# Kernel tuning notes

Hardware: AMD Instinct MI355X
Metric: run time of the kernel (lower is better)

Reference implementation:

```python
import jax, jax.numpy as jnp
import numpy as np

N_NODES = 100000
N_EDGES = 3200000
N_GRAPHS = 256
DIMS = [38, 64, 32, 16]


def setup_inputs() -> dict:
    key = jax.random.key(0)
    ks = jax.random.split(key, 16)
    x = jax.random.normal(ks[0], (N_NODES, DIMS[0]), dtype=jnp.float32)
    edge_index = jax.random.randint(ks[1], (2, N_EDGES), 0, N_NODES, dtype=jnp.int64)
    batch_vec = jnp.sort(jax.random.randint(ks[2], (N_NODES,), 0, N_GRAPHS, dtype=jnp.int64))
    inp = {"x": x, "edge_index": edge_index, "batch_vec": batch_vec}
    # Per layer l: W_rel [out,in] (with bias b [out]), W_root [out,in] (no bias)
    ki = 3
    for l in range(3):
        din, dout = DIMS[l], DIMS[l + 1]
        s = 1.0 / np.sqrt(din)
        inp[f"W_rel{l}"] = jax.random.uniform(ks[ki], (dout, din), minval=-s, maxval=s, dtype=jnp.float32); ki += 1
        inp[f"b{l}"] = jax.random.uniform(ks[ki], (dout,), minval=-s, maxval=s, dtype=jnp.float32); ki += 1
        inp[f"W_root{l}"] = jax.random.uniform(ks[ki], (dout, din), minval=-s, maxval=s, dtype=jnp.float32); ki += 1
    return inp


def _graph_conv(x, src, dst, W_rel, b, W_root):
    # sum_{j -> i} x_j, then linear (equivalent to summing transformed messages)
    agg = jax.ops.segment_sum(x[src], dst, num_segments=N_NODES)  # [N, din]
    return agg @ W_rel.T + b + x @ W_root.T


def reference(x, edge_index, batch_vec, W_rel0, b0, W_root0, W_rel1, b1, W_root1, W_rel2, b2, W_root2):
    src, dst = edge_index[0], edge_index[1]
    h = jnp.tanh(_graph_conv(x, src, dst, W_rel0, b0, W_root0))
    h = jnp.tanh(_graph_conv(h, src, dst, W_rel1, b1, W_root1))
    h = _graph_conv(h, src, dst, W_rel2, b2, W_root2)
    # global mean pool over graphs
    sums = jax.ops.segment_sum(h, batch_vec, num_segments=N_GRAPHS)  # [G, 16]
    counts = jax.ops.segment_sum(jnp.ones((N_NODES,), dtype=h.dtype), batch_vec, num_segments=N_GRAPHS)
    pooled = sums / jnp.maximum(counts, 1.0)[:, None]
    return jnp.tanh(pooled)
```

## Files before the change

### kernel.cpp

```cpp
#include <hip/hip_runtime.h>
#include <math.h>

#define N_NODES  100000
#define N_EDGES  3200000
#define N_GRAPHS 256


#define BSHIFT 8
#define NB ((N_NODES + 255) >> 8)
#define NBLK 640
#define EPB ((N_EDGES + NBLK - 1) / NBLK)

__device__ __forceinline__ float fast_tanh(float x) {
    x = fminf(20.f, fmaxf(-20.f, x));
    float e = __expf(2.f * x);
    return (e - 1.f) / (e + 1.f);
}

__device__ __forceinline__ unsigned int pack_bf2(float a, float b) {
    unsigned int ua = __float_as_uint(a);
    unsigned int ub = __float_as_uint(b);
    ua += 0x7fffu + ((ua >> 16) & 1u);
    ub += 0x7fffu + ((ub >> 16) & 1u);
    return (ua >> 16) | (ub & 0xffff0000u);
}


__global__ __launch_bounds__(256) void k_hist(const int* __restrict__ dst,
                                              int* __restrict__ bucket_cnt,
                                              int* __restrict__ blockoff) {
    __shared__ int hist[NB];
    int tid = threadIdx.x;
    int b = blockIdx.x;
    for (int i = tid; i < NB; i += 256) hist[i] = 0;
    __syncthreads();
    int lo = b * EPB;
    int hi = min(lo + EPB, N_EDGES);
    for (int e = lo + tid; e < hi; e += 256)
        atomicAdd(&hist[dst[e] >> BSHIFT], 1);
    __syncthreads();
    for (int i = tid; i < NB; i += 256) {
        int c = hist[i];
        blockoff[b * NB + i] = (c > 0) ? atomicAdd(&bucket_cnt[i], c) : 0;
    }
}

__global__ __launch_bounds__(512) void k_scan_buckets(const int* __restrict__ bucket_cnt,
                                                      int* __restrict__ bucket_base) {
    __shared__ int sd[512];
    int tid = threadIdx.x;
    int v = (tid < NB) ? bucket_cnt[tid] : 0;
    int val = v;
    sd[tid] = val;
    __syncthreads();
#pragma unroll
    for (int off = 1; off < 512; off <<= 1) {
        int t = (tid >= off) ? sd[tid - off] : 0;
        __syncthreads();
        val += t;
        sd[tid] = val;
        __syncthreads();
    }
    if (tid < NB) {
        bucket_base[tid] = val - v;
        if (tid == NB - 1) bucket_base[NB] = val;
    }
}

__global__ __launch_bounds__(256) void k_scatter_buckets(const int* __restrict__ src,
                                                         const int* __restrict__ dst,
                                                         const int* __restrict__ bucket_base,
                                                         const int* __restrict__ blockoff,
                                                         int* __restrict__ ebuf) {
    __shared__ int base[NB];
    __shared__ int cur[NB];
    int tid = threadIdx.x;
    int b = blockIdx.x;
    for (int i = tid; i < NB; i += 256) {
        base[i] = bucket_base[i] + blockoff[b * NB + i];
        cur[i] = 0;
    }
    __syncthreads();
    int lo = b * EPB;
    int hi = min(lo + EPB, N_EDGES);
    for (int e = lo + tid; e < hi; e += 256) {
        int d = dst[e];
        int bin = d >> BSHIFT;
        int r = atomicAdd(&cur[bin], 1);
        ebuf[base[bin] + r] = src[e] | ((d & 255) << 17);
    }
}

__global__ __launch_bounds__(256) void k_bucket_csr(const int* __restrict__ ebuf,
                                                    const int* __restrict__ bucket_base,
                                                    int* __restrict__ rowptr,
                                                    int* __restrict__ rowend,
                                                    int* __restrict__ elist) {
    __shared__ int cnt[256];
    __shared__ int nb[256];
    __shared__ int cur[256];
    __shared__ int sscan[256];
    int b = blockIdx.x;
    int tid = threadIdx.x;
    int e0 = bucket_base[b];
    int e1 = bucket_base[b + 1];
    cnt[tid] = 0;
    cur[tid] = 0;
    __syncthreads();
    for (int j = e0 + tid; j < e1; j += 256)
        atomicAdd(&cnt[ebuf[j] >> 17], 1);
    __syncthreads();
    int v = cnt[tid];
    int val = v;
    sscan[tid] = val;
    __syncthreads();
#pragma unroll
    for (int off = 1; off < 256; off <<= 1) {
        int t = (tid >= off) ? sscan[tid - off] : 0;
        __syncthreads();
        val += t;
        sscan[tid] = val;
        __syncthreads();
    }
    int excl = val - v;
    nb[tid] = excl;
    int node = (b << BSHIFT) + tid;
    if (node < N_NODES) {
        rowptr[node] = e0 + excl;
        rowend[node] = e0 + val;
    }
    __syncthreads();
    for (int j = e0 + tid; j < e1; j += 256) {
        int w = ebuf[j];
        int dl = w >> 17;
        int r = atomicAdd(&cur[dl], 1);
        elist[e0 + nb[dl] + r] = w & 0x1FFFF;
    }
}

__global__ __launch_bounds__(256) void k_cast_bf16(const float* __restrict__ in,
                                                   unsigned int* __restrict__ out,
                                                   int n_pairs) {
    int i = blockIdx.x * 256 + threadIdx.x;
    if (i >= n_pairs) return;
    float2 v = ((const float2*)in)[i];
    out[i] = pack_bf2(v.x, v.y);
}

template<int DIM2>
__global__ __launch_bounds__(256) void k_gather_bf16(const unsigned int* __restrict__ feat,
                                                     const int* __restrict__ rowptr,
                                                     const int* __restrict__ rowend,
                                                     const int* __restrict__ elist,
                                                     float* __restrict__ agg) {
    int idx = blockIdx.x * 256 + threadIdx.x;
    if (idx >= N_NODES * DIM2) return;
    int n = idx / DIM2;
    int p = idx - n * DIM2;
    int j = rowptr[n];
    int e = rowend[n];
    float a0 = 0.f, a1 = 0.f;
    for (; j + 3 < e; j += 4) {
        int s0 = elist[j];
        int s1 = elist[j + 1];
        int s2 = elist[j + 2];
        int s3 = elist[j + 3];
        unsigned int w0 = feat[s0 * DIM2 + p];
        unsigned int w1 = feat[s1 * DIM2 + p];
        unsigned int w2 = feat[s2 * DIM2 + p];
        unsigned int w3 = feat[s3 * DIM2 + p];
        a0 += __uint_as_float(w0 << 16);
        a1 += __uint_as_float(w0 & 0xffff0000u);
        a0 += __uint_as_float(w1 << 16);
        a1 += __uint_as_float(w1 & 0xffff0000u);
        a0 += __uint_as_float(w2 << 16);
        a1 += __uint_as_float(w2 & 0xffff0000u);
        a0 += __uint_as_float(w3 << 16);
        a1 += __uint_as_float(w3 & 0xffff0000u);
    }
    for (; j < e; ++j) {
        unsigned int w = feat[elist[j] * DIM2 + p];
        a0 += __uint_as_float(w << 16);
        a1 += __uint_as_float(w & 0xffff0000u);
    }
    agg[n * (2 * DIM2) + 2 * p]     = a0;
    agg[n * (2 * DIM2) + 2 * p + 1] = a1;
}

__global__ __launch_bounds__(256) void k_fused0(const float* __restrict__ agg,
                                                const float* __restrict__ x,
                                                const float* __restrict__ Wrel0,
                                                const float* __restrict__ b0,
                                                const float* __restrict__ Wroot0,
                                                const float* __restrict__ Wrel1,
                                                const float* __restrict__ b1,
                                                const float* __restrict__ Wroot1,
                                                unsigned int* __restrict__ y1b,
                                                float* __restrict__ r1) {
    __shared__ float sWr[64 * 40];
    __shared__ float sWt[64 * 40];
    __shared__ float sW1r[64 * 32];
    __shared__ float sW1t[64 * 32];
    __shared__ float sb0[64];
    __shared__ float sb1[32];
    int tid = threadIdx.x;
    for (int i = tid; i < 64 * 40; i += 256) {
        int o = i / 40, d = i - o * 40;
        sWr[i] = (d < 38) ? Wrel0[o * 38 + d] : 0.f;
        sWt[i] = (d < 38) ? Wroot0[o * 38 + d] : 0.f;
    }
    for (int i = tid; i < 64 * 32; i += 256) {
        int k = i >> 5, j = i & 31;
        sW1r[i] = Wrel1[j * 64 + k];
        sW1t[i] = Wroot1[j * 64 + k];
    }
    if (tid < 64) sb0[tid] = b0[tid];
    if (tid < 32) sb1[tid] = b1[tid];
    __syncthreads();

    int n = blockIdx.x * 256 + tid;
    if (n >= N_NODES) return;

    float xa[40], xx[40];
    const float2* a2 = (const float2*)(agg + (size_t)n * 38);
    const float2* x2 = (const float2*)(x + (size_t)n * 38);
#pragma unroll
    for (int i = 0; i < 19; ++i) {
        float2 va = a2[i]; xa[2 * i] = va.x; xa[2 * i + 1] = va.y;
        float2 vx = x2[i]; xx[2 * i] = vx.x; xx[2 * i + 1] = vx.y;
    }
    xa[38] = xa[39] = 0.f;
    xx[38] = xx[39] = 0.f;

    float y1[32], rr[32];
#pragma unroll
    for (int j = 0; j < 32; ++j) { y1[j] = 0.f; rr[j] = sb1[j]; }

#pragma unroll 4
    for (int o = 0; o < 64; ++o) {
        float acc = sb0[o];
        const float4* wr = (const float4*)(sWr + o * 40);
        const float4* wt = (const float4*)(sWt + o * 40);
#pragma unroll
        for (int d = 0; d < 10; ++d) {
            float4 a = wr[d], b = wt[d];
            acc += xa[4 * d] * a.x + xa[4 * d + 1] * a.y + xa[4 * d + 2] * a.z + xa[4 * d + 3] * a.w;
            acc += xx[4 * d] * b.x + xx[4 * d + 1] * b.y + xx[4 * d + 2] * b.z + xx[4 * d + 3] * b.w;
        }
        float h = fast_tanh(acc);
        const float4* w1 = (const float4*)(sW1r + o * 32);
        const float4* w2 = (const float4*)(sW1t + o * 32);
#pragma unroll
        for (int j = 0; j < 8; ++j) {
            float4 a = w1[j], b = w2[j];
            y1[4 * j]     += h * a.x; y1[4 * j + 1] += h * a.y;
            y1[4 * j + 2] += h * a.z; y1[4 * j + 3] += h * a.w;
            rr[4 * j]     += h * b.x; rr[4 * j + 1] += h * b.y;
            rr[4 * j + 2] += h * b.z; rr[4 * j + 3] += h * b.w;
        }
    }

    unsigned int* yo = y1b + (size_t)n * 16;
#pragma unroll
    for (int p = 0; p < 16; ++p) yo[p] = pack_bf2(y1[2 * p], y1[2 * p + 1]);
    float4* ro = (float4*)(r1 + (size_t)n * 32);
#pragma unroll
    for (int j = 0; j < 8; ++j) ro[j] = make_float4(rr[4 * j], rr[4 * j + 1], rr[4 * j + 2], rr[4 * j + 3]);
}

__global__ __launch_bounds__(256) void k_fused1(const float* __restrict__ agg,
                                                const float* __restrict__ r1,
                                                const float* __restrict__ Wrel2,
                                                float* __restrict__ h2,
                                                unsigned int* __restrict__ y2b)
{
    __shared__ float sW[32 * 16];
    int tid = threadIdx.x;
    for (int i = tid; i < 512; i += 256) {
        int k = i >> 4, j = i & 15;
        sW[i] = Wrel2[j * 32 + k];
    }
    __syncthreads();
    int n = blockIdx.x * 256 + tid;
    if (n >= N_NODES) return;
    const float4* a4 = (const float4*)(agg + (size_t)n * 32);
    const float4* r4 = (const float4*)(r1 + (size_t)n * 32);
    float h[32];
#pragma unroll
    for (int i = 0; i < 8; ++i) {
        float4 a = a4[i], r = r4[i];
        h[4 * i]     = fast_tanh(a.x + r.x);
        h[4 * i + 1] = fast_tanh(a.y + r.y);
        h[4 * i + 2] = fast_tanh(a.z + r.z);
        h[4 * i + 3] = fast_tanh(a.w + r.w);
    }
    float4* ho = (float4*)(h2 + (size_t)n * 32);
#pragma unroll
    for (int i = 0; i < 8; ++i) ho[i] = make_float4(h[4 * i], h[4 * i + 1], h[4 * i + 2], h[4 * i + 3]);
    float y[16];
#pragma unroll
    for (int j = 0; j < 16; ++j) y[j] = 0.f;
#pragma unroll
    for (int k = 0; k < 32; ++k) {
        const float4* w = (const float4*)(sW + k * 16);
#pragma unroll
        for (int j = 0; j < 4; ++j) {
            float4 wv = w[j];
            y[4 * j]     += h[k] * wv.x; y[4 * j + 1] += h[k] * wv.y;
            y[4 * j + 2] += h[k] * wv.z; y[4 * j + 3] += h[k] * wv.w;
        }
    }
    unsigned int* yo = y2b + (size_t)n * 8;
#pragma unroll
    for (int p = 0; p < 8; ++p) yo[p] = pack_bf2(y[2 * p], y[2 * p + 1]);
}

__global__ __launch_bounds__(256) void k_graph_start(const int* __restrict__ batch,
                                                     int* __restrict__ gstart) {
    int i = blockIdx.x * 256 + threadIdx.x;
    if (i >= N_NODES) return;
    int g = batch[i];
    int gp = (i == 0) ? -1 : batch[i - 1];
    for (int gg = gp + 1; gg <= g; ++gg) gstart[gg] = i;
    if (i == N_NODES - 1)
        for (int gg = g + 1; gg <= N_GRAPHS; ++gg) gstart[gg] = N_NODES;
}

__global__ __launch_bounds__(256) void k_pool(const float* __restrict__ agg,
                                              const float* __restrict__ h2,
                                              const int* __restrict__ gstart,
                                              float* __restrict__ psum)
{
    __shared__ float part[4][48];
    int g = blockIdx.x;
    int wave = threadIdx.x >> 6;
    int lane = threadIdx.x & 63;
    int s = gstart[g], e = gstart[g + 1];
    if (lane < 48) {
        float a0 = 0.f, a1 = 0.f;
        if (lane < 16) {
            int n = s + wave;
            for (; n + 4 < e; n += 8) {
                a0 += agg[n * 16 + lane];
                a1 += agg[(n + 4) * 16 + lane];
            }
            if (n < e) a0 += agg[n * 16 + lane];
        } else {
            int d = lane - 16;
            int n = s + wave;
            for (; n + 4 < e; n += 8) {
                a0 += h2[n * 32 + d];
                a1 += h2[(n + 4) * 32 + d];
            }
            if (n < e) a0 += h2[n * 32 + d];
        }
        part[wave][lane] = a0 + a1;
    }
    __syncthreads();
    if (threadIdx.x < 48)
        psum[g * 48 + threadIdx.x] = part[0][threadIdx.x] + part[1][threadIdx.x]
                                   + part[2][threadIdx.x] + part[3][threadIdx.x];
}

__global__ __launch_bounds__(256) void k_finalize2(const float* __restrict__ psum,
                                                   const float* __restrict__ Wroot,
                                                   const float* __restrict__ b,
                                                   const int* __restrict__ gstart,
                                                   float* __restrict__ out) {
    __shared__ float sW[16 * 32];
    __shared__ float sb[16];
    int tid = threadIdx.x;
    for (int i = tid; i < 16 * 32; i += 256) sW[i] = Wroot[i];
    if (tid < 16) sb[tid] = b[tid];
    __syncthreads();
    int idx = blockIdx.x * 256 + tid;
    if (idx >= N_GRAPHS * 16) return;
    int g = idx >> 4;
    int o = idx & 15;
    float cnt = (float)(gstart[g + 1] - gstart[g]);
    const float* p = psum + g * 48;
    float acc = p[o] + cnt * sb[o];
#pragma unroll
    for (int k = 0; k < 32; ++k) acc += p[16 + k] * sW[o * 32 + k];
    out[idx] = fast_tanh(acc / fmaxf(cnt, 1.f));
}

extern "C" void kernel_launch(void* const* d_in, const int* in_sizes, int n_in,
                              void* d_out, int out_size, void* d_ws, size_t ws_size,
                              hipStream_t stream) {
    const float* x      = (const float*)d_in[0];
    const int*   eidx   = (const int*)d_in[1];
    const int*   src    = eidx;
    const int*   dst    = eidx + N_EDGES;
    const int*   batch  = (const int*)d_in[2];
    const float* Wrel0  = (const float*)d_in[3];
    const float* b0     = (const float*)d_in[4];
    const float* Wroot0 = (const float*)d_in[5];
    const float* Wrel1  = (const float*)d_in[6];
    const float* b1     = (const float*)d_in[7];
    const float* Wroot1 = (const float*)d_in[8];
    const float* Wrel2  = (const float*)d_in[9];
    const float* b2     = (const float*)d_in[10];
    const float* Wroot2 = (const float*)d_in[11];
    float* out = (float*)d_out;

    float* ws   = (float*)d_ws;
    float* agg  = ws;
    float* r1   = agg + (size_t)N_NODES * 38;
    float* h2   = r1  + (size_t)N_NODES * 32;
    unsigned int* ybuf = (unsigned int*)(h2 + (size_t)N_NODES * 32);
    float* psum = (float*)(ybuf + (size_t)N_NODES * 16);
    int* rowptr      = (int*)(psum + N_GRAPHS * 48);
    int* rowend      = rowptr + N_NODES;
    int* gstart      = rowend + N_NODES;
    int* bucket_cnt  = gstart + 260;
    int* bucket_base = bucket_cnt + 400;
    int* blockoff    = bucket_base + 400;
    int* elist       = blockoff + NBLK * NB;
    int* ebuf        = (int*)h2;
    unsigned int* xb = (unsigned int*)r1;

    k_cast_bf16<<<(N_NODES * 19 + 255) / 256, 256, 0, stream>>>(x, xb, N_NODES * 19);

    hipMemsetAsync(bucket_cnt, 0, sizeof(int) * NB, stream);
    k_hist<<<NBLK, 256, 0, stream>>>(dst, bucket_cnt, blockoff);
    k_scan_buckets<<<1, 512, 0, stream>>>(bucket_cnt, bucket_base);
    k_scatter_buckets<<<NBLK, 256, 0, stream>>>(src, dst, bucket_base, blockoff, ebuf);
    k_bucket_csr<<<NB, 256, 0, stream>>>(ebuf, bucket_base, rowptr, rowend, elist);
    k_graph_start<<<(N_NODES + 255) / 256, 256, 0, stream>>>(batch, gstart);

    k_gather_bf16<19><<<(N_NODES * 19 + 255) / 256, 256, 0, stream>>>(xb, rowptr, rowend, elist, agg);
    k_fused0<<<(N_NODES + 255) / 256, 256, 0, stream>>>(agg, x, Wrel0, b0, Wroot0,
                                                        Wrel1, b1, Wroot1, ybuf, r1);

    k_gather_bf16<16><<<(N_NODES * 16 + 255) / 256, 256, 0, stream>>>(ybuf, rowptr, rowend, elist, agg);
    k_fused1<<<(N_NODES + 255) / 256, 256, 0, stream>>>(agg, r1, Wrel2, h2, ybuf);

    k_gather_bf16<8><<<(N_NODES * 8 + 255) / 256, 256, 0, stream>>>(ybuf, rowptr, rowend, elist, agg);

    k_pool<<<N_GRAPHS, 256, 0, stream>>>(agg, h2, gstart, psum);
    k_finalize2<<<(N_GRAPHS * 16 + 255) / 256, 256, 0, stream>>>(psum, Wroot2, b2, gstart, out);
}
```

Before: 364.2 us.

## Use packed fp16 dot products in fused layer-0/1 kernel and split outputs across half-waves

Rewrites the fused layer-0/1 node kernel so that weights and node features are held as packed fp16 pairs and accumulated with the v_dot2 fp32-accumulate instruction. Each thread now handles two nodes. The two half-waves split the hidden outputs, exchange tanh activations with a cross-lane shuffle, and then split the layer-1 outputs. This is meant to halve the FMA count and the LDS footprint in what was a compute-bound per-node matmul, at the cost of fp16 rounding of the inputs, weights and activations. It also doubles the number of histogram/scatter blocks used in CSR construction.

After: 353.1 us. 1.03x faster.

```diff
diff --git a/kernel.cpp b/kernel.cpp
--- a/kernel.cpp
+++ b/kernel.cpp
@@ -8,8 +8,11 @@
 
 #define BSHIFT 8
 #define NB ((N_NODES + 255) >> 8)
-#define NBLK 640
+#define NBLK 1280
 #define EPB ((N_EDGES + NBLK - 1) / NBLK)
+
+typedef _Float16 f16;
+typedef _Float16 f16x2 __attribute__((ext_vector_type(2)));
 
 __device__ __forceinline__ float fast_tanh(float x) {
     x = fminf(20.f, fmaxf(-20.f, x));
@@ -23,6 +26,20 @@
     ua += 0x7fffu + ((ua >> 16) & 1u);
     ub += 0x7fffu + ((ub >> 16) & 1u);
     return (ua >> 16) | (ub & 0xffff0000u);
+}
+
+__device__ __forceinline__ f16x2 u2h(unsigned int u) { union { unsigned int u; f16x2 h; } c; c.u = u; return c.h; }
+__device__ __forceinline__ unsigned int h2u(f16x2 h) { union { unsigned int u; f16x2 h; } c; c.h = h; return c.u; }
+__device__ __forceinline__ unsigned int mkh2(float a, float b) {
+    f16x2 v; v.x = (f16)a; v.y = (f16)b; return h2u(v);
+}
+
+__device__ __forceinline__ float fdot2f(f16x2 a, f16x2 b, float c) {
+#if __has_builtin(__builtin_amdgcn_fdot2)
+    return __builtin_amdgcn_fdot2(a, b, c, false);
+#else
+    return c + (float)a.x * (float)b.x + (float)a.y * (float)b.y;
+#endif
 }
 
 
@@ -197,75 +214,156 @@
                                                 const float* __restrict__ Wroot1,
                                                 unsigned int* __restrict__ y1b,
                                                 float* __restrict__ r1) {
-    __shared__ float sWr[64 * 40];
-    __shared__ float sWt[64 * 40];
-    __shared__ float sW1r[64 * 32];
-    __shared__ float sW1t[64 * 32];
+    __shared__ unsigned int sWr[64 * 20];
+    __shared__ unsigned int sWt[64 * 20];
+    __shared__ unsigned int sW1r[32 * 32];
+    __shared__ unsigned int sW1t[32 * 32];
     __shared__ float sb0[64];
     __shared__ float sb1[32];
     int tid = threadIdx.x;
-    for (int i = tid; i < 64 * 40; i += 256) {
-        int o = i / 40, d = i - o * 40;
-        sWr[i] = (d < 38) ? Wrel0[o * 38 + d] : 0.f;
-        sWt[i] = (d < 38) ? Wroot0[o * 38 + d] : 0.f;
-    }
-    for (int i = tid; i < 64 * 32; i += 256) {
-        int k = i >> 5, j = i & 31;
-        sW1r[i] = Wrel1[j * 64 + k];
-        sW1t[i] = Wroot1[j * 64 + k];
+    for (int i = tid; i < 64 * 20; i += 256) {
+        int o = i / 20, d = i - o * 20;
+        float a0 = (2 * d     < 38) ? Wrel0[o * 38 + 2 * d]     : 0.f;
+        float a1 = (2 * d + 1 < 38) ? Wrel0[o * 38 + 2 * d + 1] : 0.f;
+        float t0 = (2 * d     < 38) ? Wroot0[o * 38 + 2 * d]     : 0.f;
+        float t1 = (2 * d + 1 < 38) ? Wroot0[o * 38 + 2 * d + 1] : 0.f;
+        sWr[i] = mkh2(a0, a1);
+        sWt[i] = mkh2(t0, t1);
+    }
+    for (int i = tid; i < 32 * 32; i += 256) {
+        int op = i >> 5, j = i & 31;
+        sW1r[i] = mkh2(Wrel1[j * 64 + 2 * op], Wrel1[j * 64 + 2 * op + 1]);
+        sW1t[i] = mkh2(Wroot1[j * 64 + 2 * op], Wroot1[j * 64 + 2 * op + 1]);
     }
     if (tid < 64) sb0[tid] = b0[tid];
     if (tid < 32) sb1[tid] = b1[tid];
     __syncthreads();
 
-    int n = blockIdx.x * 256 + tid;
-    if (n >= N_NODES) return;
-
-    float xa[40], xx[40];
-    const float2* a2 = (const float2*)(agg + (size_t)n * 38);
-    const float2* x2 = (const float2*)(x + (size_t)n * 38);
-#pragma unroll
-    for (int i = 0; i < 19; ++i) {
-        float2 va = a2[i]; xa[2 * i] = va.x; xa[2 * i + 1] = va.y;
-        float2 vx = x2[i]; xx[2 * i] = vx.x; xx[2 * i + 1] = vx.y;
-    }
-    xa[38] = xa[39] = 0.f;
-    xx[38] = xx[39] = 0.f;
-
-    float y1[32], rr[32];
-#pragma unroll
-    for (int j = 0; j < 32; ++j) { y1[j] = 0.f; rr[j] = sb1[j]; }
-
-#pragma unroll 4
-    for (int o = 0; o < 64; ++o) {
-        float acc = sb0[o];
-        const float4* wr = (const float4*)(sWr + o * 40);
-        const float4* wt = (const float4*)(sWt + o * 40);
-#pragma unroll
-        for (int d = 0; d < 10; ++d) {
-            float4 a = wr[d], b = wt[d];
-            acc += xa[4 * d] * a.x + xa[4 * d + 1] * a.y + xa[4 * d + 2] * a.z + xa[4 * d + 3] * a.w;
-            acc += xx[4 * d] * b.x + xx[4 * d + 1] * b.y + xx[4 * d + 2] * b.z + xx[4 * d + 3] * b.w;
+    int lane = tid & 63;
+    int ph = lane & 31;
+    int sh = lane >> 5;
+    int n0 = blockIdx.x * 256 + (tid >> 6) * 64 + 2 * ph;
+    if (n0 >= N_NODES) return;
+    int n1 = n0 + 1;
+
+    unsigned int xa0[20], xx0[20], xa1[20], xx1[20];
+    {
+        const float2* A0 = (const float2*)(agg + (size_t)n0 * 38);
+        const float2* X0 = (const float2*)(x   + (size_t)n0 * 38);
+        const float2* A1 = (const float2*)(agg + (size_t)n1 * 38);
+        const float2* X1 = (const float2*)(x   + (size_t)n1 * 38);
+#pragma unroll
+        for (int i = 0; i < 19; ++i) {
+            float2 v;
+            v = A0[i]; xa0[i] = mkh2(v.x, v.y);
+            v = X0[i]; xx0[i] = mkh2(v.x, v.y);
+            v = A1[i]; xa1[i] = mkh2(v.x, v.y);
+            v = X1[i]; xx1[i] = mkh2(v.x, v.y);
         }
-        float h = fast_tanh(acc);
-        const float4* w1 = (const float4*)(sW1r + o * 32);
-        const float4* w2 = (const float4*)(sW1t + o * 32);
-#pragma unroll
-        for (int j = 0; j < 8; ++j) {
-            float4 a = w1[j], b = w2[j];
-            y1[4 * j]     += h * a.x; y1[4 * j + 1] += h * a.y;
-            y1[4 * j + 2] += h * a.z; y1[4 * j + 3] += h * a.w;
-            rr[4 * j]     += h * b.x; rr[4 * j + 1] += h * b.y;
-            rr[4 * j + 2] += h * b.z; rr[4 * j + 3] += h * b.w;
+        xa0[19] = 0; xx0[19] = 0; xa1[19] = 0; xx1[19] = 0;
+    }
+
+    unsigned int hp0[16], hp1[16];
+    int obase = sh * 32;
+#pragma unroll
+    for (int i = 0; i < 16; ++i) {
+        float h00 = 0.f, h01 = 0.f, h10 = 0.f, h11 = 0.f;
+#pragma unroll
+        for (int par = 0; par < 2; ++par) {
+            int o = obase + 2 * i + par;
+            float c0 = sb0[o], c1 = 0.f, c2 = 0.f, c3 = 0.f;
+            float d0 = sb0[o], d1 = 0.f, d2 = 0.f, d3 = 0.f;
+            const uint4* wr = (const uint4*)(sWr + o * 20);
+            const uint4* wt = (const uint4*)(sWt + o * 20);
+#pragma unroll
+            for (int q = 0; q < 5; ++q) {
+                uint4 w = wr[q];
+                c0 = fdot2f(u2h(xa0[4 * q + 0]), u2h(w.x), c0);
+                c1 = fdot2f(u2h(xa0[4 * q + 1]), u2h(w.y), c1);
+                c2 = fdot2f(u2h(xa0[4 * q + 2]), u2h(w.z), c2);
+                c3 = fdot2f(u2h(xa0[4 * q + 3]), u2h(w.w), c3);
+                d0 = fdot2f(u2h(xa1[4 * q + 0]), u2h(w.x), d0);
+                d1 = fdot2f(u2h(xa1[4 * q + 1]), u2h(w.y), d1);
+                d2 = fdot2f(u2h(xa1[4 * q + 2]), u2h(w.z), d2);
+                d3 = fdot2f(u2h(xa1[4 * q + 3]), u2h(w.w), d3);
+                uint4 v = wt[q];
+                c0 = fdot2f(u2h(xx0[4 * q + 0]), u2h(v.x), c0);
+                c1 = fdot2f(u2h(xx0[4 * q + 1]), u2h(v.y), c1);
+                c2 = fdot2f(u2h(xx0[4 * q + 2]), u2h(v.z), c2);
+                c3 = fdot2f(u2h(xx0[4 * q + 3]), u2h(v.w), c3);
+                d0 = fdot2f(u2h(xx1[4 * q + 0]), u2h(v.x), d0);
+                d1 = fdot2f(u2h(xx1[4 * q + 1]), u2h(v.y), d1);
+                d2 = fdot2f(u2h(xx1[4 * q + 2]), u2h(v.z), d2);
+                d3 = fdot2f(u2h(xx1[4 * q + 3]), u2h(v.w), d3);
+            }
+            float hA = fast_tanh(c0 + c1 + c2 + c3);
+            float hB = fast_tanh(d0 + d1 + d2 + d3);
+            if (par == 0) { h00 = hA; h10 = hB; }
+            else          { h01 = hA; h11 = hB; }
         }
-    }
-
-    unsigned int* yo = y1b + (size_t)n * 16;
-#pragma unroll
-    for (int p = 0; p < 16; ++p) yo[p] = pack_bf2(y1[2 * p], y1[2 * p + 1]);
-    float4* ro = (float4*)(r1 + (size_t)n * 32);
-#pragma unroll
-    for (int j = 0; j < 8; ++j) ro[j] = make_float4(rr[4 * j], rr[4 * j + 1], rr[4 * j + 2], rr[4 * j + 3]);
+        hp0[i] = mkh2(h00, h01);
+        hp1[i] = mkh2(h10, h11);
+    }
+
+    unsigned int H0[32], H1[32];
+#pragma unroll
+    for (int i = 0; i < 16; ++i) {
+        unsigned int g0 = (unsigned int)__shfl_xor((int)hp0[i], 32);
+        unsigned int g1 = (unsigned int)__shfl_xor((int)hp1[i], 32);
+        if (sh == 0) { H0[i] = hp0[i]; H0[16 + i] = g0; H1[i] = hp1[i]; H1[16 + i] = g1; }
+        else         { H0[i] = g0; H0[16 + i] = hp0[i]; H1[i] = g1; H1[16 + i] = hp1[i]; }
+    }
+
+    int jb = sh * 16;
+    float y0[16], r0[16], y1v[16], r1v[16];
+#pragma unroll
+    for (int j = 0; j < 16; ++j) {
+        y0[j] = 0.f; y1v[j] = 0.f;
+        float bb = sb1[jb + j];
+        r0[j] = bb; r1v[j] = bb;
+    }
+#pragma unroll
+    for (int op = 0; op < 32; ++op) {
+        f16x2 h0 = u2h(H0[op]);
+        f16x2 h1 = u2h(H1[op]);
+        const uint4* w1 = (const uint4*)(sW1r + op * 32 + jb);
+        const uint4* w2 = (const uint4*)(sW1t + op * 32 + jb);
+#pragma unroll
+        for (int q = 0; q < 4; ++q) {
+            uint4 a = w1[q], b = w2[q];
+            y0[4 * q + 0] = fdot2f(h0, u2h(a.x), y0[4 * q + 0]);
+            y0[4 * q + 1] = fdot2f(h0, u2h(a.y), y0[4 * q + 1]);
+            y0[4 * q + 2] = fdot2f(h0, u2h(a.z), y0[4 * q + 2]);
+            y0[4 * q + 3] = fdot2f(h0, u2h(a.w), y0[4 * q + 3]);
+            y1v[4 * q + 0] = fdot2f(h1, u2h(a.x), y1v[4 * q + 0]);
+            y1v[4 * q + 1] = fdot2f(h1, u2h(a.y), y1v[4 * q + 1]);
+            y1v[4 * q + 2] = fdot2f(h1, u2h(a.z), y1v[4 * q + 2]);
+            y1v[4 * q + 3] = fdot2f(h1, u2h(a.w), y1v[4 * q + 3]);
+            r0[4 * q + 0] = fdot2f(h0, u2h(b.x), r0[4 * q + 0]);
+            r0[4 * q + 1] = fdot2f(h0, u2h(b.y), r0[4 * q + 1]);
+            r0[4 * q + 2] = fdot2f(h0, u2h(b.z), r0[4 * q + 2]);
+            r0[4 * q + 3] = fdot2f(h0, u2h(b.w), r0[4 * q + 3]);
+            r1v[4 * q + 0] = fdot2f(h1, u2h(b.x), r1v[4 * q + 0]);
+            r1v[4 * q + 1] = fdot2f(h1, u2h(b.y), r1v[4 * q + 1]);
+            r1v[4 * q + 2] = fdot2f(h1, u2h(b.z), r1v[4 * q + 2]);
+            r1v[4 * q + 3] = fdot2f(h1, u2h(b.w), r1v[4 * q + 3]);
+        }
+    }
+
+    unsigned int* yo0 = y1b + (size_t)n0 * 16 + (jb >> 1);
+    unsigned int* yo1 = y1b + (size_t)n1 * 16 + (jb >> 1);
+#pragma unroll
+    for (int p = 0; p < 8; ++p) {
+        yo0[p] = pack_bf2(y0[2 * p], y0[2 * p + 1]);
+        yo1[p] = pack_bf2(y1v[2 * p], y1v[2 * p + 1]);
+    }
+    float4* ro0 = (float4*)(r1 + (size_t)n0 * 32 + jb);
+    float4* ro1 = (float4*)(r1 + (size_t)n1 * 32 + jb);
+#pragma unroll
+    for (int q = 0; q < 4; ++q) {
+        ro0[q] = make_float4(r0[4 * q], r0[4 * q + 1], r0[4 * q + 2], r0[4 * q + 3]);
+        ro1[q] = make_float4(r1v[4 * q], r1v[4 * q + 1], r1v[4 * q + 2], r1v[4 * q + 3]);
+    }
 }
 
 __global__ __launch_bounds__(256) void k_fused1(const float* __restrict__ agg,
@@ -416,7 +514,7 @@
     int* bucket_cnt  = gstart + 260;
     int* bucket_base = bucket_cnt + 400;
     int* blockoff    = bucket_base + 400;
-    int* elist       = blockoff + NBLK * NB;
+    int* elist       = blockoff + (size_t)NBLK * NB;
     int* ebuf        = (int*)h2;
     unsigned int* xb = (unsigned int*)r1;
 
```
